# Kernel tuning notes

Hardware: AMD Instinct MI355X
Metric: run time of the kernel (lower is better)

The kernel has to match this reference:

```python
import jax, jax.numpy as jnp
import numpy as np

N = 262144   # occupied voxels
H = 64       # channels
G = 128      # dense grid extent per axis (coords in [0, G))
K = 27       # 3x3x3 kernel offsets


def _build_neighbor_map():
    rng = np.random.default_rng(0)
    lin = rng.choice(G ** 3, size=N, replace=False).astype(np.int64)
    coords = np.stack(np.unravel_index(lin, (G, G, G)), axis=1)  # [N,3]
    table = np.full(G ** 3, N, dtype=np.int32)  # sentinel N -> zero row
    table[lin] = np.arange(N, dtype=np.int32)
    offs = np.array([(dx, dy, dz) for dx in (-1, 0, 1)
                     for dy in (-1, 0, 1) for dz in (-1, 0, 1)], dtype=np.int64)
    nbr = np.full((N, K), N, dtype=np.int32)
    for k in range(K):
        nc = coords + offs[k]
        ok = np.all((nc >= 0) & (nc < G), axis=1)
        nl = nc[ok, 0] * G * G + nc[ok, 1] * G + nc[ok, 2]
        nbr[ok, k] = table[nl]
    return nbr


def setup_inputs() -> dict:
    key = jax.random.key(0)
    k1, k2, k3 = jax.random.split(key, 3)
    scale = 1.0 / np.sqrt(K * H)  # ME-style fan-in init scale
    x = jax.random.normal(k1, (N, H), dtype=jnp.float32)
    Wa = jax.random.normal(k2, (K, H, H), dtype=jnp.float32) * scale
    Wb = jax.random.normal(k3, (K, H, H), dtype=jnp.float32) * scale
    nbr = jnp.asarray(_build_neighbor_map())
    return {"x": x, "Wa": Wa, "Wb": Wb, "nbr": nbr}


def _sparse_conv(feats, W, nbr):
    # gather -> GEMM -> accumulate, per kernel offset (missing neighbors hit zero row)
    fpad = jnp.concatenate([feats, jnp.zeros((1, feats.shape[1]), feats.dtype)], axis=0)
    out = jnp.zeros((feats.shape[0], W.shape[2]), feats.dtype)
    for k in range(W.shape[0]):
        out = out + fpad[nbr[:, k]] @ W[k]
    return out


def reference(x, Wa, Wb, nbr):
    out = _sparse_conv(x, Wa, nbr)          # spconva
    out = jax.nn.relu(out)                  # MinkowskiReLU
    out = _sparse_conv(out, Wb, nbr)        # spconvb
    return out + x                          # residual add
```

## Files before the change

kernel.cpp:

```cpp
#include <hip/hip_runtime.h>


#define N_ROWS 262144
#define HCH    64
#define KOFF   27
#define CHUNK  3

typedef unsigned short u16;
typedef __attribute__((ext_vector_type(8))) short short8;
typedef __attribute__((ext_vector_type(4))) float f32x4;

__device__ __forceinline__ u16 f2bf(float f) {
    unsigned u = __builtin_bit_cast(unsigned, f);
    unsigned r = (u + 0x7FFFu + ((u >> 16) & 1u)) >> 16;
    return (u16)r;
}
__device__ __forceinline__ float bf2f(u16 h) {
    return __builtin_bit_cast(float, (unsigned)h << 16);
}
__device__ __forceinline__ unsigned pack2(float a, float b) {
    return (unsigned)f2bf(a) | ((unsigned)f2bf(b) << 16);
}

__global__ void prep_all(const float* __restrict__ x, u16* __restrict__ xb,
                         u16* __restrict__ yb,
                         const float* __restrict__ Wa, const float* __restrict__ Wb,
                         u16* __restrict__ Wta, u16* __restrict__ Wtb,
                         const int* __restrict__ nbr, int* __restrict__ nbrT) {
    const int b = blockIdx.x;
    if (b < 8193) {
        long gid = (long)b * 256 + threadIdx.x;
        const long total = (long)N_ROWS * HCH / 8;
        if (gid < total) {
            const float4* s = (const float4*)(x + gid * 8);
            float4 a = s[0], c = s[1];
            uint4 v;
            v.x = pack2(a.x, a.y); v.y = pack2(a.z, a.w);
            v.z = pack2(c.x, c.y); v.w = pack2(c.z, c.w);
            *(uint4*)(xb + gid * 8) = v;
        } else if (gid < total + HCH / 8) {
            long c = gid - total;
            uint4 z; z.x = 0; z.y = 0; z.z = 0; z.w = 0;
            *(uint4*)(xb + (long)N_ROWS * HCH + c * 8) = z;
            *(uint4*)(yb + (long)N_ROWS * HCH + c * 8) = z;
        }
    } else if (b < 9057) {
        int gid = (b - 8193) * 256 + threadIdx.x;
        const int total = KOFF * HCH * HCH;
        const float* src; u16* dst; int e;
        if (gid < total)          { src = Wa; dst = Wta; e = gid; }
        else if (gid < 2 * total) { src = Wb; dst = Wtb; e = gid - total; }
        else return;
        int k = e >> 12, i = (e >> 6) & 63, j = e & 63;
        dst[(k << 12) + (j << 6) + i] = f2bf(src[e]);
    } else {
        __shared__ int t[32 * 27];
        const int rowbase = (b - 9057) * 32;
        for (int e = threadIdx.x; e < 32 * 27; e += 256)
            t[e] = nbr[(size_t)rowbase * KOFF + e];
        __syncthreads();
        for (int e = threadIdx.x; e < 32 * 27; e += 256) {
            int k = e >> 5, r = e & 31;
            nbrT[(size_t)k * N_ROWS + rowbase + r] = t[r * KOFF + k];
        }
    }
}

template <bool FIRST>
__global__ __launch_bounds__(256, 2) void conv_kernel(
    const u16* __restrict__ xg,
    const u16* __restrict__ Wt,
    const int* __restrict__ nb,
    u16* __restrict__ ybf,
    float* __restrict__ outf,
    const u16* __restrict__ residb)
{
    __shared__ uint4 Wlds4[CHUNK * 512];
    u16*   Wsh = (u16*)Wlds4;
    float* Fsh = (float*)Wlds4;

    const int tid  = threadIdx.x;
    const int wave = tid >> 6;
    const int lane = tid & 63;
    const int m    = lane & 15;
    const int q    = lane >> 4;
    const int base = blockIdx.x * 256 + wave * 64;

    int row[4];
#pragma unroll
    for (int t = 0; t < 4; t++) row[t] = base + t * 16 + m;

    auto ld_idx = [&](int k, int t) -> int {
        return nb[(size_t)k * N_ROWS + row[t]];
    };

    auto ldA = [&](int idx, short8& a0, short8& a1) {
        short8 z = {0, 0, 0, 0, 0, 0, 0, 0};
        a0 = z; a1 = z;
        if (idx != N_ROWS) {
            const u16* ar = xg + (size_t)idx * HCH + q * 8;
            a0 = *(const short8*)ar;
            a1 = *(const short8*)(ar + 32);
        }
    };

    f32x4 acc[4][4];
#pragma unroll
    for (int t = 0; t < 4; t++)
#pragma unroll
        for (int jt = 0; jt < 4; jt++)
            acc[t][jt] = (f32x4){0.f, 0.f, 0.f, 0.f};

    int i0[4], i1[4], idxRing[2][4];
#pragma unroll
    for (int t = 0; t < 4; t++) i0[t] = ld_idx(0, t);
#pragma unroll
    for (int t = 0; t < 4; t++) i1[t] = ld_idx(1, t);
#pragma unroll
    for (int t = 0; t < 4; t++) idxRing[0][t] = ld_idx(2, t);
#pragma unroll
    for (int t = 0; t < 4; t++) idxRing[1][t] = ld_idx(3, t);

    short8 Aring[3][4][2];
#pragma unroll
    for (int t = 0; t < 4; t++) ldA(i0[t], Aring[0][t][0], Aring[0][t][1]);
#pragma unroll
    for (int t = 0; t < 4; t++) ldA(i1[t], Aring[1][t][0], Aring[1][t][1]);

#pragma unroll
    for (int c = 0; c < KOFF / CHUNK; c++) {
        __syncthreads();
        const uint4* wg = (const uint4*)(Wt + c * CHUNK * 4096);
#pragma unroll
        for (int e = tid; e < CHUNK * 512; e += 256) {
            uint4 v = wg[e];
            int s = e >> 9, rem = e & 511, j = rem >> 3, cc = rem & 7;
            Wlds4[s * 512 + j * 8 + (cc ^ (j & 7))] = v;
        }
        __syncthreads();

#pragma unroll
        for (int s = 0; s < CHUNK; s++) {
            const int kk  = c * CHUNK + s;
            const int par = kk & 1;
            const int cur = kk % 3;
            const int nxt = (kk + 2) % 3;

#pragma unroll
            for (int t = 0; t < 4; t++)
                ldA(idxRing[par][t], Aring[nxt][t][0], Aring[nxt][t][1]);
            const int k4 = (kk + 4 < KOFF) ? kk + 4 : KOFF - 1;
#pragma unroll
            for (int t = 0; t < 4; t++) idxRing[par][t] = ld_idx(k4, t);

            const u16* bs = Wsh + s * 4096;
            short8 B0[4], B1[4];
#pragma unroll
            for (int jt = 0; jt < 4; jt++) {
                int j = jt * 16 + m;
                B0[jt] = *(const short8*)(bs + j * 64 + ((q    ) ^ (m & 7)) * 8);
                B1[jt] = *(const short8*)(bs + j * 64 + ((q + 4) ^ (m & 7)) * 8);
            }

#pragma unroll
            for (int t = 0; t < 4; t++)
#pragma unroll
                for (int jt = 0; jt < 4; jt++)
                    acc[t][jt] = __builtin_amdgcn_mfma_f32_16x16x32_bf16(
                        Aring[cur][t][0], B0[jt], acc[t][jt], 0, 0, 0);
#pragma unroll
            for (int t = 0; t < 4; t++)
#pragma unroll
                for (int jt = 0; jt < 4; jt++)
                    acc[t][jt] = __builtin_amdgcn_mfma_f32_16x16x32_bf16(
                        Aring[cur][t][1], B1[jt], acc[t][jt], 0, 0, 0);
        }
    }

    float* sl = Fsh + wave * (16 * 68);
    const int r = lane & 15;
    const int h = lane >> 4;
#pragma unroll
    for (int t = 0; t < 4; t++) {
        __syncthreads();
#pragma unroll
        for (int jt = 0; jt < 4; jt++)
#pragma unroll
            for (int rr = 0; rr < 4; rr++)
                sl[(q * 4 + rr) * 68 + jt * 16 + m] = acc[t][jt][rr];
        __syncthreads();

        float4 v0 = *(const float4*)&sl[r * 68 + h * 16 + 0];
        float4 v1 = *(const float4*)&sl[r * 68 + h * 16 + 4];
        float4 v2 = *(const float4*)&sl[r * 68 + h * 16 + 8];
        float4 v3 = *(const float4*)&sl[r * 68 + h * 16 + 12];
        const size_t grow = (size_t)(base + t * 16 + r);
        if (FIRST) {
            uint4 o0, o1;
            o0.x = pack2(fmaxf(v0.x, 0.f), fmaxf(v0.y, 0.f));
            o0.y = pack2(fmaxf(v0.z, 0.f), fmaxf(v0.w, 0.f));
            o0.z = pack2(fmaxf(v1.x, 0.f), fmaxf(v1.y, 0.f));
            o0.w = pack2(fmaxf(v1.z, 0.f), fmaxf(v1.w, 0.f));
            o1.x = pack2(fmaxf(v2.x, 0.f), fmaxf(v2.y, 0.f));
            o1.y = pack2(fmaxf(v2.z, 0.f), fmaxf(v2.w, 0.f));
            o1.z = pack2(fmaxf(v3.x, 0.f), fmaxf(v3.y, 0.f));
            o1.w = pack2(fmaxf(v3.z, 0.f), fmaxf(v3.w, 0.f));
            uint4* dst = (uint4*)(ybf + grow * HCH + h * 16);
            dst[0] = o0; dst[1] = o1;
        } else {
            const uint4* rb = (const uint4*)(residb + grow * HCH + h * 16);
            uint4 r0 = rb[0], r1 = rb[1];
            float4 o;
            float* op = outf + grow * HCH + h * 16;
            o.x = v0.x + bf2f((u16)(r0.x & 0xFFFF));
            o.y = v0.y + bf2f((u16)(r0.x >> 16));
            o.z = v0.z + bf2f((u16)(r0.y & 0xFFFF));
            o.w = v0.w + bf2f((u16)(r0.y >> 16));
            *(float4*)(op + 0) = o;
            o.x = v1.x + bf2f((u16)(r0.z & 0xFFFF));
            o.y = v1.y + bf2f((u16)(r0.z >> 16));
            o.z = v1.z + bf2f((u16)(r0.w & 0xFFFF));
            o.w = v1.w + bf2f((u16)(r0.w >> 16));
            *(float4*)(op + 4) = o;
            o.x = v2.x + bf2f((u16)(r1.x & 0xFFFF));
            o.y = v2.y + bf2f((u16)(r1.x >> 16));
            o.z = v2.z + bf2f((u16)(r1.y & 0xFFFF));
            o.w = v2.w + bf2f((u16)(r1.y >> 16));
            *(float4*)(op + 8) = o;
            o.x = v3.x + bf2f((u16)(r1.z & 0xFFFF));
            o.y = v3.y + bf2f((u16)(r1.z >> 16));
            o.z = v3.z + bf2f((u16)(r1.w & 0xFFFF));
            o.w = v3.w + bf2f((u16)(r1.w >> 16));
            *(float4*)(op + 12) = o;
        }
    }
}

extern "C" void kernel_launch(void* const* d_in, const int* in_sizes, int n_in,
                              void* d_out, int out_size, void* d_ws, size_t ws_size,
                              hipStream_t stream) {
    const float* x   = (const float*)d_in[0];
    const float* Wa  = (const float*)d_in[1];
    const float* Wb  = (const float*)d_in[2];
    const int*   nbr = (const int*)d_in[3];
    float* out = (float*)d_out;

    char* ws = (char*)d_ws;
    const size_t xb_bytes = (size_t)(N_ROWS + 1) * HCH * sizeof(u16);
    const size_t w_bytes  = (size_t)KOFF * HCH * HCH * sizeof(u16);
    u16* xb  = (u16*)ws;
    u16* yb  = (u16*)(ws + xb_bytes);
    u16* Wta = (u16*)(ws + 2 * xb_bytes);
    u16* Wtb = (u16*)(ws + 2 * xb_bytes + w_bytes);
    int* nbrT = (int*)(ws + 2 * xb_bytes + 2 * w_bytes);

    prep_all<<<17249, 256, 0, stream>>>(x, xb, yb, Wa, Wb, Wta, Wtb, nbr, nbrT);
    conv_kernel<true ><<<N_ROWS / 256, 256, 0, stream>>>(xb, Wta, nbrT, yb, nullptr, nullptr);
    conv_kernel<false><<<N_ROWS / 256, 256, 0, stream>>>(yb, Wtb, nbrT, nullptr, out, xb);
}
```

Before: 297.1 us.

## Split K-dimension across wave pairs with LDS reduction, halve rows per block

Each block now covers 128 rows instead of 256. Pairs of waves split the 64-channel input (K) dimension in half, so each wave issues half the MFMAs and holds half the A/B fragments, and the two partial accumulators are summed through LDS in the epilogue. This cuts register pressure, which allows launch bounds of 3 blocks per CU and doubles the grid for more latency hiding on the gathers. The cost is that each block loads the full weights for half as many rows, doubling weight traffic into LDS, plus an extra LDS reduction step.

After: 513.2 us. 72.7% more time.

```diff
diff --git a/kernel.cpp b/kernel.cpp
--- a/kernel.cpp
+++ b/kernel.cpp
@@ -67,7 +67,7 @@
 }
 
 template <bool FIRST>
-__global__ __launch_bounds__(256, 2) void conv_kernel(
+__global__ __launch_bounds__(256, 3) void conv_kernel(
     const u16* __restrict__ xg,
     const u16* __restrict__ Wt,
     const int* __restrict__ nb,
@@ -82,9 +82,11 @@
     const int tid  = threadIdx.x;
     const int wave = tid >> 6;
     const int lane = tid & 63;
+    const int g    = wave >> 1;
+    const int h    = wave & 1;
     const int m    = lane & 15;
     const int q    = lane >> 4;
-    const int base = blockIdx.x * 256 + wave * 64;
+    const int base = blockIdx.x * 128 + g * 64;
 
     int row[4];
 #pragma unroll
@@ -94,13 +96,12 @@
         return nb[(size_t)k * N_ROWS + row[t]];
     };
 
-    auto ldA = [&](int idx, short8& a0, short8& a1) {
+    auto ldA = [&](int idx, short8& a0) {
         short8 z = {0, 0, 0, 0, 0, 0, 0, 0};
-        a0 = z; a1 = z;
+        a0 = z;
         if (idx != N_ROWS) {
-            const u16* ar = xg + (size_t)idx * HCH + q * 8;
+            const u16* ar = xg + (size_t)idx * HCH + h * 32 + q * 8;
             a0 = *(const short8*)ar;
-            a1 = *(const short8*)(ar + 32);
         }
     };
 
@@ -121,11 +122,11 @@
 #pragma unroll
     for (int t = 0; t < 4; t++) idxRing[1][t] = ld_idx(3, t);
 
-    short8 Aring[3][4][2];
-#pragma unroll
-    for (int t = 0; t < 4; t++) ldA(i0[t], Aring[0][t][0], Aring[0][t][1]);
-#pragma unroll
-    for (int t = 0; t < 4; t++) ldA(i1[t], Aring[1][t][0], Aring[1][t][1]);
+    short8 Aring[3][4];
+#pragma unroll
+    for (int t = 0; t < 4; t++) ldA(i0[t], Aring[0][t]);
+#pragma unroll
+    for (int t = 0; t < 4; t++) ldA(i1[t], Aring[1][t]);
 
 #pragma unroll
     for (int c = 0; c < KOFF / CHUNK; c++) {
@@ -148,18 +149,17 @@
 
 #pragma unroll
             for (int t = 0; t < 4; t++)
-                ldA(idxRing[par][t], Aring[nxt][t][0], Aring[nxt][t][1]);
+                ldA(idxRing[par][t], Aring[nxt][t]);
             const int k4 = (kk + 4 < KOFF) ? kk + 4 : KOFF - 1;
 #pragma unroll
             for (int t = 0; t < 4; t++) idxRing[par][t] = ld_idx(k4, t);
 
             const u16* bs = Wsh + s * 4096;
-            short8 B0[4], B1[4];
+            short8 Bf[4];
 #pragma unroll
             for (int jt = 0; jt < 4; jt++) {
                 int j = jt * 16 + m;
-                B0[jt] = *(const short8*)(bs + j * 64 + ((q    ) ^ (m & 7)) * 8);
-                B1[jt] = *(const short8*)(bs + j * 64 + ((q + 4) ^ (m & 7)) * 8);
+                Bf[jt] = *(const short8*)(bs + j * 64 + ((q + 4 * h) ^ (m & 7)) * 8);
             }
 
 #pragma unroll
@@ -167,19 +167,15 @@
 #pragma unroll
                 for (int jt = 0; jt < 4; jt++)
                     acc[t][jt] = __builtin_amdgcn_mfma_f32_16x16x32_bf16(
-                        Aring[cur][t][0], B0[jt], acc[t][jt], 0, 0, 0);
-#pragma unroll
-            for (int t = 0; t < 4; t++)
-#pragma unroll
-                for (int jt = 0; jt < 4; jt++)
-                    acc[t][jt] = __builtin_amdgcn_mfma_f32_16x16x32_bf16(
-                        Aring[cur][t][1], B1[jt], acc[t][jt], 0, 0, 0);
+                        Aring[cur][t], Bf[jt], acc[t][jt], 0, 0, 0);
         }
     }
 
-    float* sl = Fsh + wave * (16 * 68);
-    const int r = lane & 15;
-    const int h = lane >> 4;
+    float* sl  = Fsh + wave * (16 * 68);
+    float* sl0 = Fsh + (g * 2 + 0) * (16 * 68);
+    float* sl1 = Fsh + (g * 2 + 1) * (16 * 68);
+    const int r  = lane & 15;
+    const int c8 = (lane >> 4) + h * 4;
 #pragma unroll
     for (int t = 0; t < 4; t++) {
         __syncthreads();
@@ -190,48 +186,39 @@
                 sl[(q * 4 + rr) * 68 + jt * 16 + m] = acc[t][jt][rr];
         __syncthreads();
 
-        float4 v0 = *(const float4*)&sl[r * 68 + h * 16 + 0];
-        float4 v1 = *(const float4*)&sl[r * 68 + h * 16 + 4];
-        float4 v2 = *(const float4*)&sl[r * 68 + h * 16 + 8];
-        float4 v3 = *(const float4*)&sl[r * 68 + h * 16 + 12];
+        const int fo = r * 68 + c8 * 8;
+        float4 p0 = *(const float4*)&sl0[fo];
+        float4 p1 = *(const float4*)&sl0[fo + 4];
+        float4 q0 = *(const float4*)&sl1[fo];
+        float4 q1 = *(const float4*)&sl1[fo + 4];
+        float4 v0, v1;
+        v0.x = p0.x + q0.x; v0.y = p0.y + q0.y;
+        v0.z = p0.z + q0.z; v0.w = p0.w + q0.w;
+        v1.x = p1.x + q1.x; v1.y = p1.y + q1.y;
+        v1.z = p1.z + q1.z; v1.w = p1.w + q1.w;
+
         const size_t grow = (size_t)(base + t * 16 + r);
         if (FIRST) {
-            uint4 o0, o1;
-            o0.x = pack2(fmaxf(v0.x, 0.f), fmaxf(v0.y, 0.f));
-            o0.y = pack2(fmaxf(v0.z, 0.f), fmaxf(v0.w, 0.f));
-            o0.z = pack2(fmaxf(v1.x, 0.f), fmaxf(v1.y, 0.f));
-            o0.w = pack2(fmaxf(v1.z, 0.f), fmaxf(v1.w, 0.f));
-            o1.x = pack2(fmaxf(v2.x, 0.f), fmaxf(v2.y, 0.f));
-            o1.y = pack2(fmaxf(v2.z, 0.f), fmaxf(v2.w, 0.f));
-            o1.z = pack2(fmaxf(v3.x, 0.f), fmaxf(v3.y, 0.f));
-            o1.w = pack2(fmaxf(v3.z, 0.f), fmaxf(v3.w, 0.f));
-            uint4* dst = (uint4*)(ybf + grow * HCH + h * 16);
-            dst[0] = o0; dst[1] = o1;
+            uint4 o;
+            o.x = pack2(fmaxf(v0.x, 0.f), fmaxf(v0.y, 0.f));
+            o.y = pack2(fmaxf(v0.z, 0.f), fmaxf(v0.w, 0.f));
+            o.z = pack2(fmaxf(v1.x, 0.f), fmaxf(v1.y, 0.f));
+            o.w = pack2(fmaxf(v1.z, 0.f), fmaxf(v1.w, 0.f));
+            *(uint4*)(ybf + grow * HCH + c8 * 8) = o;
         } else {
-            const uint4* rb = (const uint4*)(residb + grow * HCH + h * 16);
-            uint4 r0 = rb[0], r1 = rb[1];
+            const uint4 rv = *(const uint4*)(residb + grow * HCH + c8 * 8);
+            float* op = outf + grow * HCH + c8 * 8;
             float4 o;
-            float* op = outf + grow * HCH + h * 16;
-            o.x = v0.x + bf2f((u16)(r0.x & 0xFFFF));
-            o.y = v0.y + bf2f((u16)(r0.x >> 16));
-            o.z = v0.z + bf2f((u16)(r0.y & 0xFFFF));
-            o.w = v0.w + bf2f((u16)(r0.y >> 16));
+            o.x = v0.x + bf2f((u16)(rv.x & 0xFFFF));
+            o.y = v0.y + bf2f((u16)(rv.x >> 16));
+            o.z = v0.z + bf2f((u16)(rv.y & 0xFFFF));
+            o.w = v0.w + bf2f((u16)(rv.y >> 16));
             *(float4*)(op + 0) = o;
-            o.x = v1.x + bf2f((u16)(r0.z & 0xFFFF));
-            o.y = v1.y + bf2f((u16)(r0.z >> 16));
-            o.z = v1.z + bf2f((u16)(r0.w & 0xFFFF));
-            o.w = v1.w + bf2f((u16)(r0.w >> 16));
+            o.x = v1.x + bf2f((u16)(rv.z & 0xFFFF));
+            o.y = v1.y + bf2f((u16)(rv.z >> 16));
+            o.z = v1.z + bf2f((u16)(rv.w & 0xFFFF));
+            o.w = v1.w + bf2f((u16)(rv.w >> 16));
             *(float4*)(op + 4) = o;
-            o.x = v2.x + bf2f((u16)(r1.x & 0xFFFF));
-            o.y = v2.y + bf2f((u16)(r1.x >> 16));
-            o.z = v2.z + bf2f((u16)(r1.y & 0xFFFF));
-            o.w = v2.w + bf2f((u16)(r1.y >> 16));
-            *(float4*)(op + 8) = o;
-            o.x = v3.x + bf2f((u16)(r1.z & 0xFFFF));
-            o.y = v3.y + bf2f((u16)(r1.z >> 16));
-            o.z = v3.z + bf2f((u16)(r1.w & 0xFFFF));
-            o.w = v3.w + bf2f((u16)(r1.w >> 16));
-            *(float4*)(op + 12) = o;
         }
     }
 }
@@ -255,6 +242,6 @@
     int* nbrT = (int*)(ws + 2 * xb_bytes + 2 * w_bytes);
 
     prep_all<<<17249, 256, 0, stream>>>(x, xb, yb, Wa, Wb, Wta, Wtb, nbr, nbrT);
-    conv_kernel<true ><<<N_ROWS / 256, 256, 0, stream>>>(xb, Wta, nbrT, yb, nullptr, nullptr);
-    conv_kernel<false><<<N_ROWS / 256, 256, 0, stream>>>(yb, Wtb, nbrT, nullptr, out, xb);
-}
+    conv_kernel<true ><<<N_ROWS / 128, 256, 0, stream>>>(xb, Wta, nbrT, yb, nullptr, nullptr);
+    conv_kernel<false><<<N_ROWS / 128, 256, 0, stream>>>(yb, Wtb, nbrT, nullptr, out, xb);
+}
```

## Double-buffer weight chunks in LDS with register prefetch of next chunk

Applied to the files above, without the earlier changes.

Weight chunks are now loaded from global into registers one chunk ahead and written into an alternate LDS buffer after the current chunk's MFMAs. This replaces the two barriers per chunk with one lightweight barrier, so weight fetch latency overlaps with compute. In exchange LDS use doubles (48KB per block), which may limit occupancy, and 24 extra VGPRs hold the prefetched data.

Measured after the change: 308.9 us. 1.04x slower.

```diff
diff --git a/kernel.cpp b/kernel.cpp
--- a/kernel.cpp
+++ b/kernel.cpp
@@ -20,6 +20,12 @@
 }
 __device__ __forceinline__ unsigned pack2(float a, float b) {
     return (unsigned)f2bf(a) | ((unsigned)f2bf(b) << 16);
+}
+
+__device__ __forceinline__ void sync_lds() {
+    asm volatile("s_waitcnt lgkmcnt(0)" ::: "memory");
+    __builtin_amdgcn_s_barrier();
+    asm volatile("" ::: "memory");
 }
 
 __global__ void prep_all(const float* __restrict__ x, u16* __restrict__ xb,
@@ -75,8 +81,7 @@
     float* __restrict__ outf,
     const u16* __restrict__ residb)
 {
-    __shared__ uint4 Wlds4[CHUNK * 512];
-    u16*   Wsh = (u16*)Wlds4;
+    __shared__ uint4 Wlds4[2 * CHUNK * 512];
     float* Fsh = (float*)Wlds4;
 
     const int tid  = threadIdx.x;
@@ -104,6 +109,12 @@
         }
     };
 
+    auto wWrite = [&](uint4* wb, int i, uint4 v) {
+        int e = tid + i * 256;
+        int s = e >> 9, rem = e & 511, j = rem >> 3, cc = rem & 7;
+        wb[s * 512 + j * 8 + (cc ^ (j & 7))] = v;
+    };
+
     f32x4 acc[4][4];
 #pragma unroll
     for (int t = 0; t < 4; t++)
@@ -111,6 +122,13 @@
         for (int jt = 0; jt < 4; jt++)
             acc[t][jt] = (f32x4){0.f, 0.f, 0.f, 0.f};
 
+    uint4 wreg[6];
+    {
+        const uint4* wg = (const uint4*)Wt;
+#pragma unroll
+        for (int i = 0; i < 6; i++) wreg[i] = wg[tid + i * 256];
+    }
+
     int i0[4], i1[4], idxRing[2][4];
 #pragma unroll
     for (int t = 0; t < 4; t++) i0[t] = ld_idx(0, t);
@@ -128,17 +146,19 @@
     for (int t = 0; t < 4; t++) ldA(i1[t], Aring[1][t][0], Aring[1][t][1]);
 
 #pragma unroll
+    for (int i = 0; i < 6; i++) wWrite(Wlds4, i, wreg[i]);
+    sync_lds();
+
+#pragma unroll
     for (int c = 0; c < KOFF / CHUNK; c++) {
-        __syncthreads();
-        const uint4* wg = (const uint4*)(Wt + c * CHUNK * 4096);
-#pragma unroll
-        for (int e = tid; e < CHUNK * 512; e += 256) {
-            uint4 v = wg[e];
-            int s = e >> 9, rem = e & 511, j = rem >> 3, cc = rem & 7;
-            Wlds4[s * 512 + j * 8 + (cc ^ (j & 7))] = v;
-        }
-        __syncthreads();
-
+        const int buf = c & 1;
+        if (c + 1 < KOFF / CHUNK) {
+            const uint4* wg = (const uint4*)(Wt + (c + 1) * CHUNK * 4096);
+#pragma unroll
+            for (int i = 0; i < 6; i++) wreg[i] = wg[tid + i * 256];
+        }
+
+        const u16* WshC = (const u16*)(Wlds4 + buf * (CHUNK * 512));
 #pragma unroll
         for (int s = 0; s < CHUNK; s++) {
             const int kk  = c * CHUNK + s;
@@ -153,7 +173,7 @@
 #pragma unroll
             for (int t = 0; t < 4; t++) idxRing[par][t] = ld_idx(k4, t);
 
-            const u16* bs = Wsh + s * 4096;
+            const u16* bs = WshC + s * 4096;
             short8 B0[4], B1[4];
 #pragma unroll
             for (int jt = 0; jt < 4; jt++) {
@@ -174,6 +194,13 @@
                 for (int jt = 0; jt < 4; jt++)
                     acc[t][jt] = __builtin_amdgcn_mfma_f32_16x16x32_bf16(
                         Aring[cur][t][1], B1[jt], acc[t][jt], 0, 0, 0);
+        }
+
+        if (c + 1 < KOFF / CHUNK) {
+            uint4* wb = Wlds4 + (buf ^ 1) * (CHUNK * 512);
+#pragma unroll
+            for (int i = 0; i < 6; i++) wWrite(wb, i, wreg[i]);
+            sync_lds();
         }
     }
 
```
